# Kernel optimization log

Hardware: AMD Instinct MI355X
Metric: run time of the kernel (lower is better)

## Reference

```python
import jax, jax.numpy as jnp
import numpy as np

N = 50000       # num_nodes
E = 1_600_000   # num_edges (avg degree 32)
F_IN, HID, F_OUT = 128, 128, 64


def setup_inputs() -> dict:
    key = jax.random.key(0)
    k0, k1, k2, k3 = jax.random.split(key, 4)
    x = jax.random.normal(k0, (1, N, F_IN), dtype=jnp.float32)
    edge_index = jax.random.randint(k1, (2, E), 0, N, dtype=jnp.int32)
    # GCNConv weights (glorot-ish scale) and zero biases
    W1 = jax.random.normal(k2, (F_IN, HID), dtype=jnp.float32) / np.float32(np.sqrt(F_IN))
    b1 = jnp.zeros((HID,), dtype=jnp.float32)
    W2 = jax.random.normal(k3, (HID, F_OUT), dtype=jnp.float32) / np.float32(np.sqrt(HID))
    b2 = jnp.zeros((F_OUT,), dtype=jnp.float32)
    return {"x": x, "edge_index": edge_index, "W1": W1, "b1": b1, "W2": W2, "b2": b2}


def _gcn_layer(h, src, dst, norm, W, b, n):
    # linear transform then symmetric-normalized scatter-add aggregation
    h = h @ W                              # [N, F_out]
    msg = h[src] * norm[:, None]           # [E+N, F_out] gathered messages
    agg = jax.ops.segment_sum(msg, dst, num_segments=n)
    return agg + b


def reference(x, edge_index, W1, b1, W2, b2):
    xn = x[0]                              # [N, F_in] node feature matrix
    n = xn.shape[0]
    src, dst = edge_index[0], edge_index[1]
    # add self-loops (GCNConv default)
    loops = jnp.arange(n, dtype=src.dtype)
    src = jnp.concatenate([src, loops])
    dst = jnp.concatenate([dst, loops])
    # symmetric normalization: deg^-1/2[src] * deg^-1/2[dst] (deg >= 1 w/ self-loops)
    deg = jax.ops.segment_sum(jnp.ones(dst.shape, dtype=xn.dtype), dst, num_segments=n)
    dinv = jax.lax.rsqrt(deg)
    norm = dinv[src] * dinv[dst]
    h = jax.nn.relu(_gcn_layer(xn, src, dst, norm, W1, b1, n))
    out = jax.nn.relu(_gcn_layer(h, src, dst, norm, W2, b2, n))
    return out
```

## Files before the change

### kernel.cpp

```cpp
#include <hip/hip_runtime.h>
#include <hip/hip_fp16.h>


#define TILE 8192
#define BIN_CAP 2560

typedef _Float16 half8 __attribute__((ext_vector_type(8)));
typedef float floatx4 __attribute__((ext_vector_type(4)));

__device__ __forceinline__ void accs8(float* ax, const uint4& u, float d) {
    float2 f;
    f = __half22float2(*(const __half2*)&u.x); ax[0] = fmaf(d, f.x, ax[0]); ax[1] = fmaf(d, f.y, ax[1]);
    f = __half22float2(*(const __half2*)&u.y); ax[2] = fmaf(d, f.x, ax[2]); ax[3] = fmaf(d, f.y, ax[3]);
    f = __half22float2(*(const __half2*)&u.z); ax[4] = fmaf(d, f.x, ax[4]); ax[5] = fmaf(d, f.y, ax[5]);
    f = __half22float2(*(const __half2*)&u.w); ax[6] = fmaf(d, f.x, ax[6]); ax[7] = fmaf(d, f.y, ax[7]);
}

__device__ __forceinline__ void acc8(float* ax, const uint4& u) {
    float2 f;
    f = __half22float2(*(const __half2*)&u.x); ax[0] += f.x; ax[1] += f.y;
    f = __half22float2(*(const __half2*)&u.y); ax[2] += f.x; ax[3] += f.y;
    f = __half22float2(*(const __half2*)&u.z); ax[4] += f.x; ax[5] += f.y;
    f = __half22float2(*(const __half2*)&u.w); ax[6] += f.x; ax[7] += f.y;
}

template <int COLS>
__global__ __launch_bounds__(512) void bin_gemm(
        const int* __restrict__ src, const int* __restrict__ dst, int E,
        int nbins, int numTiles,
        int* __restrict__ binCnt, unsigned* __restrict__ recs,
        const float* __restrict__ Xv, const float* __restrict__ W,
        __half* __restrict__ Y, int N) {
    constexpr int LDA = 136;
    __shared__ __align__(16) _Float16 smem[(64 + COLS) * LDA];
    int tid = threadIdx.x;

    if (blockIdx.x < numTiles) {
        int* cnt = (int*)smem;
        int* gbase = cnt + nbins;
        for (int i = tid; i < nbins; i += 512) cnt[i] = 0;
        __syncthreads();

        int t0 = blockIdx.x * TILE;
        int tEnd = min(t0 + TILE, E);

        for (int e = t0 + tid; e < tEnd; e += 512)
            atomicAdd(&cnt[dst[e] >> 6], 1);
        __syncthreads();

        for (int i = tid; i < nbins; i += 512) {
            int c = cnt[i];
            gbase[i] = (c > 0) ? atomicAdd(&binCnt[i], c) : 0;
            cnt[i] = 0;
        }
        __syncthreads();

        for (int e = t0 + tid; e < tEnd; e += 512) {
            int d = dst[e];
            int s = src[e];
            int b = d >> 6;
            int r = atomicAdd(&cnt[b], 1);
            int g = gbase[b] + r;
            if (g < BIN_CAP)
                recs[(size_t)b * BIN_CAP + g] = ((unsigned)(d & 63) << 16) | (unsigned)s;
        }
        return;
    }

    int bid = blockIdx.x - numTiles;
    _Float16* aT = smem;
    _Float16* bT = smem + 64 * LDA;
    int lane = tid & 63, wave = tid >> 6;
    int row0 = bid * 64;

    for (int i = tid * 4; i < 64 * 128; i += 2048) {
        int r = i >> 7, k = i & 127;
        int gr = row0 + r;
        float4 v = make_float4(0.f, 0.f, 0.f, 0.f);
        if (gr < N) v = *(const float4*)&Xv[(size_t)gr * 128 + k];
        __half2 p0 = __floats2half2_rn(v.x, v.y);
        __half2 p1 = __floats2half2_rn(v.z, v.w);
        *(uint2*)&aT[r * LDA + k] = make_uint2(*(uint*)&p0, *(uint*)&p1);
    }
    for (int i = tid; i < 128 * COLS; i += 512) {
        int k = i / COLS, n = i % COLS;
        bT[n * LDA + k] = (_Float16)W[i];
    }
    __syncthreads();

    constexpr int NT = COLS / 16;
    int m = lane & 15, q = lane >> 4;
    floatx4 acc[NT];
    if (wave < 4) {
        #pragma unroll
        for (int t = 0; t < NT; t++) acc[t] = (floatx4){0.f, 0.f, 0.f, 0.f};
        const _Float16* arow = &aT[(wave * 16 + m) * LDA + q * 8];
        #pragma unroll
        for (int ks = 0; ks < 4; ks++) {
            half8 af = *(const half8*)&arow[ks * 32];
            #pragma unroll
            for (int t = 0; t < NT; t++) {
                half8 bf = *(const half8*)&bT[(t * 16 + m) * LDA + ks * 32 + q * 8];
                acc[t] = __builtin_amdgcn_mfma_f32_16x16x32_f16(af, bf, acc[t], 0, 0, 0);
            }
        }
    }
    __syncthreads();

    if (wave < 4) {
        #pragma unroll
        for (int t = 0; t < NT; t++)
            #pragma unroll
            for (int r = 0; r < 4; r++)
                aT[(wave * 16 + q * 4 + r) * LDA + t * 16 + m] = (_Float16)acc[t][r];
    }
    __syncthreads();

    for (int i = tid; i < 64 * (COLS / 2); i += 512) {
        int r = i / (COLS / 2), c = i % (COLS / 2);
        int gr = row0 + r;
        if (gr < N)
            ((uint*)Y)[(size_t)gr * (COLS / 2) + c] = *(uint*)&aT[r * LDA + c * 2];
    }
}

__global__ __launch_bounds__(512) void sort_bins(const unsigned* __restrict__ recs,
                                                 const int* __restrict__ binCnt,
                                                 unsigned short* __restrict__ sortedG,
                                                 int* __restrict__ startG,
                                                 float* __restrict__ dinv, int N) {
    __shared__ unsigned short sorted[BIN_CAP];
    __shared__ int c64[64];
    __shared__ int start[65];
    __shared__ int cursor[64];
    int b = blockIdx.x, tid = threadIdx.x;
    int lane = tid & 63, wave = tid >> 6;

    if (tid < 64) c64[tid] = 0;
    __syncthreads();
    int cnt = min(binCnt[b], BIN_CAP);
    const unsigned* bin = recs + (size_t)b * BIN_CAP;

    for (int i = tid; i < cnt; i += 512)
        atomicAdd(&c64[bin[i] >> 16], 1);
    __syncthreads();

    if (wave == 0) {
        int c = c64[lane];
        int v = c;
        #pragma unroll
        for (int off = 1; off < 64; off <<= 1) {
            int t = __shfl_up(v, off);
            if (lane >= off) v += t;
        }
        start[lane] = v - c;
        cursor[lane] = v - c;
        startG[b * 65 + lane] = v - c;
        if (lane == 63) { start[64] = v; startG[b * 65 + 64] = v; }
        int n = (b << 6) + lane;
        if (n < N) dinv[n] = rsqrtf((float)(c + 1));
    }
    __syncthreads();

    for (int i = tid; i < cnt; i += 512) {
        unsigned r = bin[i];
        int pos = atomicAdd(&cursor[r >> 16], 1);
        sorted[pos] = (unsigned short)(r & 0xFFFFu);
    }
    __syncthreads();
    unsigned short* sg = sortedG + (size_t)b * BIN_CAP;
    for (int i = tid; i < cnt; i += 512) sg[i] = sorted[i];
}

__global__ __launch_bounds__(512) void agg_gemm_fused(
        const __half* __restrict__ G,
        const unsigned short* __restrict__ sortedG,
        const int* __restrict__ startG,
        const float* __restrict__ dinv,
        const float* __restrict__ bias,
        const float* __restrict__ W2,
        __half* __restrict__ Y2, int N) {
    constexpr int LDH = 136;
    __shared__ unsigned short buf[BIN_CAP];
    __shared__ int st[65];
    __shared__ __align__(16) _Float16 hT[64 * LDH];
    __shared__ __align__(16) _Float16 bT[64 * LDH];

    int b = blockIdx.x;
    int tid = threadIdx.x, lane = tid & 63, wave = tid >> 6;
    int ql = lane & 15, quad = lane >> 4;

    if (tid < 65) st[tid] = startG[b * 65 + tid];
    __syncthreads();
    int cnt = st[64];
    const unsigned short* sg = sortedG + (size_t)b * BIN_CAP;
    for (int i = tid; i < cnt; i += 512) buf[i] = sg[i];
    for (int i = tid; i < 128 * 64; i += 512) {
        int k = i >> 6, n = i & 63;
        bT[n * LDH + k] = (_Float16)W2[i];
    }
    __syncthreads();

    float bb[8];
    #pragma unroll
    for (int k = 0; k < 4; k++) {
        float2 t = *(const float2*)&bias[ql * 8 + k * 2];
        bb[k * 2] = t.x; bb[k * 2 + 1] = t.y;
    }

    for (int rr = 0; rr < 8; rr++) {
        int row = wave * 8 + rr;
        int n = (b << 6) + row;
        if (n >= N) {
            if (quad == 0) {
                uint4 z = make_uint4(0, 0, 0, 0);
                *(uint4*)&hT[row * LDH + ql * 8] = z;
            }
            continue;
        }
        int jst = st[row], jen = st[row + 1];

        float ax[8] = {};
        int j = jst + quad;
        for (; j + 4 < jen; j += 8) {
            int sA = buf[j], sB = buf[j + 4];
            uint4 uA = *(const uint4*)&G[(size_t)sA * 128 + ql * 8];
            uint4 uB = *(const uint4*)&G[(size_t)sB * 128 + ql * 8];
            float dA = dinv[sA], dB = dinv[sB];
            accs8(ax, uA, dA);
            accs8(ax, uB, dB);
        }
        for (; j < jen; j += 4) {
            int s = buf[j];
            uint4 u = *(const uint4*)&G[(size_t)s * 128 + ql * 8];
            accs8(ax, u, dinv[s]);
        }
        #pragma unroll
        for (int k = 0; k < 8; k++) {
            ax[k] += __shfl_xor(ax[k], 16);
            ax[k] += __shfl_xor(ax[k], 32);
        }
        if (quad == 0) {
            uint4 us = *(const uint4*)&G[(size_t)n * 128 + ql * 8];
            float di = dinv[n];
            accs8(ax, us, di);
            __half2 h[4];
            #pragma unroll
            for (int k = 0; k < 4; k++) {
                float o0 = fmaxf(fmaf(di, ax[k * 2],     bb[k * 2]),     0.0f);
                float o1 = fmaxf(fmaf(di, ax[k * 2 + 1], bb[k * 2 + 1]), 0.0f);
                h[k] = __floats2half2_rn(o0, o1);
            }
            *(uint4*)&hT[row * LDH + ql * 8] = *(uint4*)h;
        }
    }
    __syncthreads();

    int m = lane & 15, q = lane >> 4;
    int mt = wave & 3, nt0 = (wave >> 2) * 2;
    floatx4 acc[2] = {(floatx4){0.f, 0.f, 0.f, 0.f}, (floatx4){0.f, 0.f, 0.f, 0.f}};
    const _Float16* arow = &hT[(mt * 16 + m) * LDH + q * 8];
    #pragma unroll
    for (int ks = 0; ks < 4; ks++) {
        half8 af = *(const half8*)&arow[ks * 32];
        #pragma unroll
        for (int t = 0; t < 2; t++) {
            half8 bf = *(const half8*)&bT[((nt0 + t) * 16 + m) * LDH + ks * 32 + q * 8];
            acc[t] = __builtin_amdgcn_mfma_f32_16x16x32_f16(af, bf, acc[t], 0, 0, 0);
        }
    }
    __syncthreads();

    float dv[4];
    #pragma unroll
    for (int r = 0; r < 4; r++) {
        int gr = (b << 6) + mt * 16 + q * 4 + r;
        dv[r] = (gr < N) ? dinv[gr] : 0.0f;
    }
    #pragma unroll
    for (int t = 0; t < 2; t++)
        #pragma unroll
        for (int r = 0; r < 4; r++)
            hT[(mt * 16 + q * 4 + r) * LDH + (nt0 + t) * 16 + m] = (_Float16)(dv[r] * acc[t][r]);
    __syncthreads();

    for (int i = tid; i < 64 * 32; i += 512) {
        int r = i >> 5, c = i & 31;
        int gr = (b << 6) + r;
        if (gr < N)
            ((uint*)Y2)[(size_t)gr * 32 + c] = *(uint*)&hT[r * LDH + c * 2];
    }
}

__global__ __launch_bounds__(512) void agg_64(const __half* __restrict__ G,
                                              const unsigned short* __restrict__ sortedG,
                                              const int* __restrict__ startG,
                                              const float* __restrict__ dinv,
                                              const float* __restrict__ bias,
                                              float* __restrict__ out, int N) {
    __shared__ unsigned short buf[BIN_CAP];
    __shared__ int st[33];
    int b = blockIdx.x, half_ = blockIdx.y;
    int tid = threadIdx.x, lane = tid & 63, wave = tid >> 6;
    int ol = lane & 7, oct = lane >> 3;
    int r0 = half_ * 32;

    if (tid < 33) st[tid] = startG[b * 65 + r0 + tid];
    __syncthreads();
    int S0 = st[0], S1 = st[32];
    const unsigned short* sg = sortedG + (size_t)b * BIN_CAP;
    for (int i = tid; i < S1 - S0; i += 512) buf[i] = sg[S0 + i];
    __syncthreads();

    float bb[8];
    #pragma unroll
    for (int k = 0; k < 4; k++) {
        float2 t = *(const float2*)&bias[ol * 8 + k * 2];
        bb[k * 2] = t.x; bb[k * 2 + 1] = t.y;
    }

    for (int rr = 0; rr < 4; rr++) {
        int row = wave * 4 + rr;
        int n = (b << 6) + r0 + row;
        if (n >= N) continue;
        int jst = st[row] - S0, jen = st[row + 1] - S0;

        float ax[8] = {};
        int j = jst + oct;
        for (; j + 8 < jen; j += 16) {
            int sA = buf[j], sB = buf[j + 8];
            uint4 uA = *(const uint4*)&G[(size_t)sA * 64 + ol * 8];
            uint4 uB = *(const uint4*)&G[(size_t)sB * 64 + ol * 8];
            acc8(ax, uA);
            acc8(ax, uB);
        }
        for (; j < jen; j += 8) {
            int s = buf[j];
            uint4 u = *(const uint4*)&G[(size_t)s * 64 + ol * 8];
            acc8(ax, u);
        }
        #pragma unroll
        for (int k = 0; k < 8; k++) {
            ax[k] += __shfl_xor(ax[k], 8);
            ax[k] += __shfl_xor(ax[k], 16);
            ax[k] += __shfl_xor(ax[k], 32);
        }
        if (oct < 2) {
            uint4 us = *(const uint4*)&G[(size_t)n * 64 + ol * 8];
            acc8(ax, us);
            float di = dinv[n];
            float o[8];
            #pragma unroll
            for (int k = 0; k < 8; k++)
                o[k] = fmaxf(fmaf(di, ax[k], bb[k]), 0.0f);
            if (oct == 0)
                *(float4*)&out[(size_t)n * 64 + ol * 8] = make_float4(o[0], o[1], o[2], o[3]);
            else
                *(float4*)&out[(size_t)n * 64 + ol * 8 + 4] = make_float4(o[4], o[5], o[6], o[7]);
        }
    }
}

extern "C" void kernel_launch(void* const* d_in, const int* in_sizes, int n_in,
                              void* d_out, int out_size, void* d_ws, size_t ws_size,
                              hipStream_t stream) {
    const float* x  = (const float*)d_in[0];
    const int*   ei = (const int*)d_in[1];
    const float* W1 = (const float*)d_in[2];
    const float* b1 = (const float*)d_in[3];
    const float* W2 = (const float*)d_in[4];
    const float* b2 = (const float*)d_in[5];
    float* out = (float*)d_out;

    const int HID  = in_sizes[3];
    const int F_IN = in_sizes[2] / HID;
    const int N    = in_sizes[0] / F_IN;
    const int E    = in_sizes[1] / 2;
    (void)n_in; (void)out_size; (void)ws_size; (void)F_IN;

    const int* src = ei;
    const int* dst = ei + E;

    const int nbins = (N + 63) >> 6;

    char* p = (char*)d_ws;
    auto carve = [&](size_t bytes) { void* q = (void*)p; p += (bytes + 255) & ~(size_t)255; return q; };
    int*            binCnt  = (int*)           carve((size_t)nbins * 4);
    float*          dinv    = (float*)         carve((size_t)N * 4);
    unsigned*       recs    = (unsigned*)      carve((size_t)nbins * BIN_CAP * 4);
    unsigned short* sortedG = (unsigned short*)carve((size_t)nbins * BIN_CAP * 2);
    int*            startG  = (int*)           carve((size_t)nbins * 65 * 4);
    __half*         bufG    = (__half*)        carve((size_t)N * 128 * 2);
    __half*         bufG2   = (__half*)        carve((size_t)N * 64 * 2);

    hipMemsetAsync(binCnt, 0, (size_t)nbins * 4, stream);

    int numTiles = (E + TILE - 1) / TILE;
    int gemmGrid = (N + 63) / 64;
    bin_gemm<128><<<numTiles + gemmGrid, 512, 0, stream>>>(
        src, dst, E, nbins, numTiles, binCnt, recs, x, W1, bufG, N);

    sort_bins<<<nbins, 512, 0, stream>>>(recs, binCnt, sortedG, startG, dinv, N);

    agg_gemm_fused<<<nbins, 512, 0, stream>>>(bufG, sortedG, startG, dinv, b1, W2, bufG2, N);

    dim3 aggGrid(nbins, 2);
    agg_64<<<aggGrid, 512, 0, stream>>>(bufG2, sortedG, startG, dinv, b2, out, N);
}
```

Baseline: 205.2 us.

## Prescale layer-1 features by source dinv using a separate degree-count kernel

Adds a kernel that counts in-degrees with global atomics before the first GEMM, so the GEMM epilogue can multiply each output row by its source-side rsqrt(deg+1). The layer-1 aggregation loop then only sums the gathered fp16 rows, with no per-edge dinv gather and no FMA by it. The cost is an extra launch and a pass over E edges with about 1.6M global atomics, plus a rounding change because the scaling is applied before the fp16 conversion.

```diff
diff --git a/kernel.cpp b/kernel.cpp
--- a/kernel.cpp
+++ b/kernel.cpp
@@ -7,14 +7,6 @@
 
 typedef _Float16 half8 __attribute__((ext_vector_type(8)));
 typedef float floatx4 __attribute__((ext_vector_type(4)));
-
-__device__ __forceinline__ void accs8(float* ax, const uint4& u, float d) {
-    float2 f;
-    f = __half22float2(*(const __half2*)&u.x); ax[0] = fmaf(d, f.x, ax[0]); ax[1] = fmaf(d, f.y, ax[1]);
-    f = __half22float2(*(const __half2*)&u.y); ax[2] = fmaf(d, f.x, ax[2]); ax[3] = fmaf(d, f.y, ax[3]);
-    f = __half22float2(*(const __half2*)&u.z); ax[4] = fmaf(d, f.x, ax[4]); ax[5] = fmaf(d, f.y, ax[5]);
-    f = __half22float2(*(const __half2*)&u.w); ax[6] = fmaf(d, f.x, ax[6]); ax[7] = fmaf(d, f.y, ax[7]);
-}
 
 __device__ __forceinline__ void acc8(float* ax, const uint4& u) {
     float2 f;
@@ -24,12 +16,34 @@
     f = __half22float2(*(const __half2*)&u.w); ax[6] += f.x; ax[7] += f.y;
 }
 
+template <bool VEC>
+__global__ __launch_bounds__(512) void deg_count(const int* __restrict__ dst, int E,
+                                                 int* __restrict__ deg) {
+    if (VEC) {
+        int nv = E >> 2;
+        const int4* d4 = (const int4*)dst;
+        for (int k = blockIdx.x * 512 + threadIdx.x; k < nv; k += gridDim.x * 512) {
+            int4 d = d4[k];
+            atomicAdd(&deg[d.x], 1);
+            atomicAdd(&deg[d.y], 1);
+            atomicAdd(&deg[d.z], 1);
+            atomicAdd(&deg[d.w], 1);
+        }
+        if (blockIdx.x == 0 && (int)threadIdx.x < (E & 3))
+            atomicAdd(&deg[dst[(nv << 2) + threadIdx.x]], 1);
+    } else {
+        for (int e = blockIdx.x * 512 + threadIdx.x; e < E; e += gridDim.x * 512)
+            atomicAdd(&deg[dst[e]], 1);
+    }
+}
+
 template <int COLS>
 __global__ __launch_bounds__(512) void bin_gemm(
         const int* __restrict__ src, const int* __restrict__ dst, int E,
         int nbins, int numTiles,
         int* __restrict__ binCnt, unsigned* __restrict__ recs,
         const float* __restrict__ Xv, const float* __restrict__ W,
+        const int* __restrict__ deg,
         __half* __restrict__ Y, int N) {
     constexpr int LDA = 136;
     __shared__ __align__(16) _Float16 smem[(64 + COLS) * LDA];
@@ -108,11 +122,17 @@
     __syncthreads();
 
     if (wave < 4) {
+        float dv[4];
+        #pragma unroll
+        for (int r = 0; r < 4; r++) {
+            int gr = row0 + wave * 16 + q * 4 + r;
+            dv[r] = (gr < N) ? rsqrtf((float)(deg[gr] + 1)) : 0.0f;
+        }
         #pragma unroll
         for (int t = 0; t < NT; t++)
             #pragma unroll
             for (int r = 0; r < 4; r++)
-                aT[(wave * 16 + q * 4 + r) * LDA + t * 16 + m] = (_Float16)acc[t][r];
+                aT[(wave * 16 + q * 4 + r) * LDA + t * 16 + m] = (_Float16)(dv[r] * acc[t][r]);
     }
     __syncthreads();
 
@@ -226,14 +246,13 @@
             int sA = buf[j], sB = buf[j + 4];
             uint4 uA = *(const uint4*)&G[(size_t)sA * 128 + ql * 8];
             uint4 uB = *(const uint4*)&G[(size_t)sB * 128 + ql * 8];
-            float dA = dinv[sA], dB = dinv[sB];
-            accs8(ax, uA, dA);
-            accs8(ax, uB, dB);
+            acc8(ax, uA);
+            acc8(ax, uB);
         }
         for (; j < jen; j += 4) {
             int s = buf[j];
             uint4 u = *(const uint4*)&G[(size_t)s * 128 + ql * 8];
-            accs8(ax, u, dinv[s]);
+            acc8(ax, u);
         }
         #pragma unroll
         for (int k = 0; k < 8; k++) {
@@ -242,8 +261,8 @@
         }
         if (quad == 0) {
             uint4 us = *(const uint4*)&G[(size_t)n * 128 + ql * 8];
+            acc8(ax, us);
             float di = dinv[n];
-            accs8(ax, us, di);
             __half2 h[4];
             #pragma unroll
             for (int k = 0; k < 4; k++) {
@@ -386,6 +405,7 @@
     char* p = (char*)d_ws;
     auto carve = [&](size_t bytes) { void* q = (void*)p; p += (bytes + 255) & ~(size_t)255; return q; };
     int*            binCnt  = (int*)           carve((size_t)nbins * 4);
+    int*            deg     = (int*)           carve((size_t)N * 4);
     float*          dinv    = (float*)         carve((size_t)N * 4);
     unsigned*       recs    = (unsigned*)      carve((size_t)nbins * BIN_CAP * 4);
     unsigned short* sortedG = (unsigned short*)carve((size_t)nbins * BIN_CAP * 2);
@@ -393,12 +413,25 @@
     __half*         bufG    = (__half*)        carve((size_t)N * 128 * 2);
     __half*         bufG2   = (__half*)        carve((size_t)N * 64 * 2);
 
-    hipMemsetAsync(binCnt, 0, (size_t)nbins * 4, stream);
+    size_t zeroBytes = (size_t)((char*)dinv - (char*)binCnt);
+    hipMemsetAsync(binCnt, 0, zeroBytes, stream);
+
+    bool vec = ((reinterpret_cast<uintptr_t>(dst) & 15) == 0) && ((E & 3) == 0 || E >= 4);
+    if (vec) {
+        int nv = E >> 2;
+        int dblocks = min((nv + 511) / 512, 1024);
+        if (dblocks < 1) dblocks = 1;
+        deg_count<true><<<dblocks, 512, 0, stream>>>(dst, E, deg);
+    } else {
+        int dblocks = min((E + 511) / 512, 2048);
+        if (dblocks < 1) dblocks = 1;
+        deg_count<false><<<dblocks, 512, 0, stream>>>(dst, E, deg);
+    }
 
     int numTiles = (E + TILE - 1) / TILE;
     int gemmGrid = (N + 63) / 64;
     bin_gemm<128><<<numTiles + gemmGrid, 512, 0, stream>>>(
-        src, dst, E, nbins, numTiles, binCnt, recs, x, W1, bufG, N);
+        src, dst, E, nbins, numTiles, binCnt, recs, x, W1, deg, bufG, N);
 
     sort_bins<<<nbins, 512, 0, stream>>>(recs, binCnt, sortedG, startG, dinv, N);
 
```

Measured after the change: 275.9 us. 1.34x slower.

## Fuse GCN pipeline into a single cooperative persistent kernel with grid syncs

Applied to the files above, without the earlier changes.

Replaces the memset plus four separate launches with one cooperative kernel of nbins blocks that runs binning, the first GEMM, bin sorting, dinv-scaled store, fused aggregation+GEMM and final aggregation, separated by grid-wide syncs. The first GEMM result is held in registers across the sort phase and pre-scaled by dinv before storing, and the last aggregation uses a different wave layout. The aim is to remove launch gaps and tail effects between stages. The cost is grid-sync overhead, an occupancy requirement of 782 co-resident blocks, and lower parallelism in the final stage (one block per bin instead of two). A fallback to the old multi-kernel path is kept when cooperative launch capacity is insufficient.

```diff
diff --git a/kernel.cpp b/kernel.cpp
--- a/kernel.cpp
+++ b/kernel.cpp
@@ -1,5 +1,8 @@
 #include <hip/hip_runtime.h>
 #include <hip/hip_fp16.h>
+#include <hip/hip_cooperative_groups.h>
+
+namespace cg = cooperative_groups;
 
 
 #define TILE 8192
@@ -7,6 +10,14 @@
 
 typedef _Float16 half8 __attribute__((ext_vector_type(8)));
 typedef float floatx4 __attribute__((ext_vector_type(4)));
+
+__device__ __forceinline__ void acc8(float* ax, const uint4& u) {
+    float2 f;
+    f = __half22float2(*(const __half2*)&u.x); ax[0] += f.x; ax[1] += f.y;
+    f = __half22float2(*(const __half2*)&u.y); ax[2] += f.x; ax[3] += f.y;
+    f = __half22float2(*(const __half2*)&u.z); ax[4] += f.x; ax[5] += f.y;
+    f = __half22float2(*(const __half2*)&u.w); ax[6] += f.x; ax[7] += f.y;
+}
 
 __device__ __forceinline__ void accs8(float* ax, const uint4& u, float d) {
     float2 f;
@@ -16,16 +27,334 @@
     f = __half22float2(*(const __half2*)&u.w); ax[6] = fmaf(d, f.x, ax[6]); ax[7] = fmaf(d, f.y, ax[7]);
 }
 
-__device__ __forceinline__ void acc8(float* ax, const uint4& u) {
-    float2 f;
-    f = __half22float2(*(const __half2*)&u.x); ax[0] += f.x; ax[1] += f.y;
-    f = __half22float2(*(const __half2*)&u.y); ax[2] += f.x; ax[3] += f.y;
-    f = __half22float2(*(const __half2*)&u.z); ax[4] += f.x; ax[5] += f.y;
-    f = __half22float2(*(const __half2*)&u.w); ax[6] += f.x; ax[7] += f.y;
+__global__ __launch_bounds__(512, 8) void mega_gcn(
+        const int* __restrict__ src, const int* __restrict__ dst, int E,
+        int nbins, int numTiles,
+        int* __restrict__ binCnt, unsigned* __restrict__ recs,
+        const float* __restrict__ Xv, const float* __restrict__ W1,
+        unsigned short* __restrict__ sortedG, int* __restrict__ startG,
+        float* __restrict__ dinv,
+        const float* __restrict__ b1, const float* __restrict__ W2,
+        __half* __restrict__ bufG, __half* __restrict__ bufG2,
+        const float* __restrict__ b2, float* __restrict__ out, int N) {
+    __shared__ __align__(16) char L[40448];
+    cg::grid_group gridg = cg::this_grid();
+    int bid = blockIdx.x, tid = threadIdx.x;
+    int lane = tid & 63, wave = tid >> 6;
+
+    for (int i = bid * 512 + tid; i < nbins; i += gridDim.x * 512) binCnt[i] = 0;
+    gridg.sync();
+
+    if (bid < numTiles) {
+        int* cnt = (int*)L;
+        int* gbase = cnt + nbins;
+        for (int i = tid; i < nbins; i += 512) cnt[i] = 0;
+        __syncthreads();
+        int t0 = bid * TILE, tEnd = min(t0 + TILE, E);
+        for (int e = t0 + tid; e < tEnd; e += 512)
+            atomicAdd(&cnt[dst[e] >> 6], 1);
+        __syncthreads();
+        for (int i = tid; i < nbins; i += 512) {
+            int c = cnt[i];
+            gbase[i] = (c > 0) ? atomicAdd(&binCnt[i], c) : 0;
+            cnt[i] = 0;
+        }
+        __syncthreads();
+        for (int e = t0 + tid; e < tEnd; e += 512) {
+            int d = dst[e], s = src[e];
+            int b = d >> 6;
+            int r = atomicAdd(&cnt[b], 1);
+            int g = gbase[b] + r;
+            if (g < BIN_CAP)
+                recs[(size_t)b * BIN_CAP + g] = ((unsigned)(d & 63) << 16) | (unsigned)s;
+        }
+        __syncthreads();
+    }
+
+    int gtile = bid + (nbins - numTiles);
+    if (gtile >= nbins) gtile -= nbins;
+    int row0g = gtile * 64;
+    floatx4 accg[8];
+    #pragma unroll
+    for (int t = 0; t < 8; t++) accg[t] = (floatx4){0.f, 0.f, 0.f, 0.f};
+    {
+        _Float16* aT  = (_Float16*)L;
+        _Float16* bTh = (_Float16*)(L + 17408);
+        for (int i = tid * 4; i < 64 * 128; i += 2048) {
+            int r = i >> 7, k = i & 127;
+            int gr = row0g + r;
+            float4 v = make_float4(0.f, 0.f, 0.f, 0.f);
+            if (gr < N) v = *(const float4*)&Xv[(size_t)gr * 128 + k];
+            __half2 p0 = __floats2half2_rn(v.x, v.y);
+            __half2 p1 = __floats2half2_rn(v.z, v.w);
+            *(uint2*)&aT[r * 136 + k] = make_uint2(*(uint*)&p0, *(uint*)&p1);
+        }
+        int m = lane & 15, q = lane >> 4;
+        #pragma unroll
+        for (int h = 0; h < 2; h++) {
+            __syncthreads();
+            for (int i = tid; i < 128 * 64; i += 512) {
+                int k = i >> 6, n = i & 63;
+                bTh[n * 136 + k] = (_Float16)W1[k * 128 + h * 64 + n];
+            }
+            __syncthreads();
+            if (wave < 4) {
+                const _Float16* arow = &aT[(wave * 16 + m) * 136 + q * 8];
+                #pragma unroll
+                for (int ks = 0; ks < 4; ks++) {
+                    half8 af = *(const half8*)&arow[ks * 32];
+                    #pragma unroll
+                    for (int t = 0; t < 4; t++) {
+                        half8 bf = *(const half8*)&bTh[(t * 16 + m) * 136 + ks * 32 + q * 8];
+                        accg[h * 4 + t] = __builtin_amdgcn_mfma_f32_16x16x32_f16(
+                            af, bf, accg[h * 4 + t], 0, 0, 0);
+                    }
+                }
+            }
+        }
+    }
+    gridg.sync();
+
+    {
+        unsigned short* sorted = (unsigned short*)L;
+        int* c64    = (int*)(L + 5120);
+        int* cursor = (int*)(L + 5648);
+        if (tid < 64) c64[tid] = 0;
+        __syncthreads();
+        int cnt = min(binCnt[bid], BIN_CAP);
+        const unsigned* bin = recs + (size_t)bid * BIN_CAP;
+        for (int i = tid; i < cnt; i += 512)
+            atomicAdd(&c64[bin[i] >> 16], 1);
+        __syncthreads();
+        if (wave == 0) {
+            int c = c64[lane];
+            int v = c;
+            #pragma unroll
+            for (int off = 1; off < 64; off <<= 1) {
+                int t = __shfl_up(v, off);
+                if (lane >= off) v += t;
+            }
+            cursor[lane] = v - c;
+            startG[bid * 65 + lane] = v - c;
+            if (lane == 63) startG[bid * 65 + 64] = v;
+            int n = (bid << 6) + lane;
+            if (n < N) dinv[n] = rsqrtf((float)(c + 1));
+        }
+        __syncthreads();
+        for (int i = tid; i < cnt; i += 512) {
+            unsigned r = bin[i];
+            int pos = atomicAdd(&cursor[r >> 16], 1);
+            sorted[pos] = (unsigned short)(r & 0xFFFFu);
+        }
+        __syncthreads();
+        unsigned short* sg = sortedG + (size_t)bid * BIN_CAP;
+        for (int i = tid; i < cnt; i += 512) sg[i] = sorted[i];
+    }
+    gridg.sync();
+
+    {
+        _Float16* bounce = (_Float16*)L;
+        int m = lane & 15, q = lane >> 4;
+        if (wave < 4) {
+            float dv[4];
+            #pragma unroll
+            for (int r = 0; r < 4; r++) {
+                int gr = row0g + wave * 16 + q * 4 + r;
+                dv[r] = (gr < N) ? dinv[gr] : 0.0f;
+            }
+            #pragma unroll
+            for (int h = 0; h < 2; h++)
+                #pragma unroll
+                for (int t = 0; t < 4; t++)
+                    #pragma unroll
+                    for (int r = 0; r < 4; r++)
+                        bounce[(wave * 16 + q * 4 + r) * 136 + h * 64 + t * 16 + m] =
+                            (_Float16)(dv[r] * accg[h * 4 + t][r]);
+        }
+        __syncthreads();
+        for (int i = tid; i < 64 * 64; i += 512) {
+            int r = i >> 6, c = i & 63;
+            int gr = row0g + r;
+            if (gr < N)
+                ((uint*)bufG)[(size_t)gr * 64 + c] = *(uint*)&bounce[r * 136 + c * 2];
+        }
+    }
+    gridg.sync();
+
+    {
+        constexpr int LDH = 136;
+        unsigned short* buf = (unsigned short*)L;
+        int* st = (int*)(L + 5120);
+        _Float16* hT = (_Float16*)(L + 5408);
+        _Float16* bT = (_Float16*)(L + 22816);
+        int ql = lane & 15, quad = lane >> 4;
+
+        if (tid < 65) st[tid] = startG[bid * 65 + tid];
+        __syncthreads();
+        int cnt = st[64];
+        const unsigned short* sg = sortedG + (size_t)bid * BIN_CAP;
+        for (int i = tid; i < cnt; i += 512) buf[i] = sg[i];
+        for (int i = tid; i < 128 * 64; i += 512) {
+            int k = i >> 6, n = i & 63;
+            bT[n * LDH + k] = (_Float16)W2[i];
+        }
+        __syncthreads();
+
+        float bb[8];
+        #pragma unroll
+        for (int k = 0; k < 4; k++) {
+            float2 t = *(const float2*)&b1[ql * 8 + k * 2];
+            bb[k * 2] = t.x; bb[k * 2 + 1] = t.y;
+        }
+
+        const __half* G = bufG;
+        for (int rr = 0; rr < 8; rr++) {
+            int row = wave * 8 + rr;
+            int n = (bid << 6) + row;
+            if (n >= N) {
+                if (quad == 0) {
+                    uint4 z = make_uint4(0, 0, 0, 0);
+                    *(uint4*)&hT[row * LDH + ql * 8] = z;
+                }
+                continue;
+            }
+            int jst = st[row], jen = st[row + 1];
+            float ax[8] = {};
+            int j = jst + quad;
+            for (; j + 4 < jen; j += 8) {
+                int sA = buf[j], sB = buf[j + 4];
+                uint4 uA = *(const uint4*)&G[(size_t)sA * 128 + ql * 8];
+                uint4 uB = *(const uint4*)&G[(size_t)sB * 128 + ql * 8];
+                acc8(ax, uA);
+                acc8(ax, uB);
+            }
+            for (; j < jen; j += 4) {
+                int s = buf[j];
+                uint4 u = *(const uint4*)&G[(size_t)s * 128 + ql * 8];
+                acc8(ax, u);
+            }
+            #pragma unroll
+            for (int k = 0; k < 8; k++) {
+                ax[k] += __shfl_xor(ax[k], 16);
+                ax[k] += __shfl_xor(ax[k], 32);
+            }
+            if (quad == 0) {
+                uint4 us = *(const uint4*)&G[(size_t)n * 128 + ql * 8];
+                acc8(ax, us);
+                float di = dinv[n];
+                __half2 h[4];
+                #pragma unroll
+                for (int k = 0; k < 4; k++) {
+                    float o0 = fmaxf(fmaf(di, ax[k * 2],     bb[k * 2]),     0.0f);
+                    float o1 = fmaxf(fmaf(di, ax[k * 2 + 1], bb[k * 2 + 1]), 0.0f);
+                    h[k] = __floats2half2_rn(o0, o1);
+                }
+                *(uint4*)&hT[row * LDH + ql * 8] = *(uint4*)h;
+            }
+        }
+        __syncthreads();
+
+        int m = lane & 15, q = lane >> 4;
+        int mt = wave & 3, nt0 = (wave >> 2) * 2;
+        floatx4 acc[2] = {(floatx4){0.f, 0.f, 0.f, 0.f}, (floatx4){0.f, 0.f, 0.f, 0.f}};
+        const _Float16* arow = &hT[(mt * 16 + m) * LDH + q * 8];
+        #pragma unroll
+        for (int ks = 0; ks < 4; ks++) {
+            half8 af = *(const half8*)&arow[ks * 32];
+            #pragma unroll
+            for (int t = 0; t < 2; t++) {
+                half8 bf = *(const half8*)&bT[((nt0 + t) * 16 + m) * LDH + ks * 32 + q * 8];
+                acc[t] = __builtin_amdgcn_mfma_f32_16x16x32_f16(af, bf, acc[t], 0, 0, 0);
+            }
+        }
+        __syncthreads();
+
+        float dv[4];
+        #pragma unroll
+        for (int r = 0; r < 4; r++) {
+            int gr = (bid << 6) + mt * 16 + q * 4 + r;
+            dv[r] = (gr < N) ? dinv[gr] : 0.0f;
+        }
+        #pragma unroll
+        for (int t = 0; t < 2; t++)
+            #pragma unroll
+            for (int r = 0; r < 4; r++)
+                hT[(mt * 16 + q * 4 + r) * LDH + (nt0 + t) * 16 + m] = (_Float16)(dv[r] * acc[t][r]);
+        __syncthreads();
+
+        for (int i = tid; i < 64 * 32; i += 512) {
+            int r = i >> 5, c = i & 31;
+            int gr = (bid << 6) + r;
+            if (gr < N)
+                ((uint*)bufG2)[(size_t)gr * 32 + c] = *(uint*)&hT[r * LDH + c * 2];
+        }
+    }
+    gridg.sync();
+
+    {
+        unsigned short* buf = (unsigned short*)L;
+        int* st = (int*)(L + 5120);
+        int ol = lane & 7, oct = lane >> 3;
+
+        if (tid < 65) st[tid] = startG[bid * 65 + tid];
+        __syncthreads();
+        int cnt = st[64];
+        const unsigned short* sg = sortedG + (size_t)bid * BIN_CAP;
+        for (int i = tid; i < cnt; i += 512) buf[i] = sg[i];
+        __syncthreads();
+
+        float bb[8];
+        #pragma unroll
+        for (int k = 0; k < 4; k++) {
+            float2 t = *(const float2*)&b2[ol * 8 + k * 2];
+            bb[k * 2] = t.x; bb[k * 2 + 1] = t.y;
+        }
+
+        const __half* G = bufG2;
+        for (int rr = 0; rr < 8; rr++) {
+            int row = wave * 8 + rr;
+            int n = (bid << 6) + row;
+            if (n >= N) continue;
+            int jst = st[row], jen = st[row + 1];
+            float ax[8] = {};
+            int j = jst + oct;
+            for (; j + 8 < jen; j += 16) {
+                int sA = buf[j], sB = buf[j + 8];
+                uint4 uA = *(const uint4*)&G[(size_t)sA * 64 + ol * 8];
+                uint4 uB = *(const uint4*)&G[(size_t)sB * 64 + ol * 8];
+                acc8(ax, uA);
+                acc8(ax, uB);
+            }
+            for (; j < jen; j += 8) {
+                int s = buf[j];
+                uint4 u = *(const uint4*)&G[(size_t)s * 64 + ol * 8];
+                acc8(ax, u);
+            }
+            #pragma unroll
+            for (int k = 0; k < 8; k++) {
+                ax[k] += __shfl_xor(ax[k], 8);
+                ax[k] += __shfl_xor(ax[k], 16);
+                ax[k] += __shfl_xor(ax[k], 32);
+            }
+            if (oct < 2) {
+                uint4 us = *(const uint4*)&G[(size_t)n * 64 + ol * 8];
+                acc8(ax, us);
+                float di = dinv[n];
+                float o[8];
+                #pragma unroll
+                for (int k = 0; k < 8; k++)
+                    o[k] = fmaxf(fmaf(di, ax[k], bb[k]), 0.0f);
+                if (oct == 0)
+                    *(float4*)&out[(size_t)n * 64 + ol * 8] = make_float4(o[0], o[1], o[2], o[3]);
+                else
+                    *(float4*)&out[(size_t)n * 64 + ol * 8 + 4] = make_float4(o[4], o[5], o[6], o[7]);
+            }
+        }
+    }
 }
 
 template <int COLS>
-__global__ __launch_bounds__(512) void bin_gemm(
+__global__ __launch_bounds__(512) void fb_bin_gemm(
         const int* __restrict__ src, const int* __restrict__ dst, int E,
         int nbins, int numTiles,
         int* __restrict__ binCnt, unsigned* __restrict__ recs,
@@ -40,24 +369,19 @@
         int* gbase = cnt + nbins;
         for (int i = tid; i < nbins; i += 512) cnt[i] = 0;
         __syncthreads();
-
         int t0 = blockIdx.x * TILE;
         int tEnd = min(t0 + TILE, E);
-
         for (int e = t0 + tid; e < tEnd; e += 512)
             atomicAdd(&cnt[dst[e] >> 6], 1);
         __syncthreads();
-
         for (int i = tid; i < nbins; i += 512) {
             int c = cnt[i];
             gbase[i] = (c > 0) ? atomicAdd(&binCnt[i], c) : 0;
             cnt[i] = 0;
         }
         __syncthreads();
-
         for (int e = t0 + tid; e < tEnd; e += 512) {
-            int d = dst[e];
-            int s = src[e];
+            int d = dst[e], s = src[e];
             int b = d >> 6;
             int r = atomicAdd(&cnt[b], 1);
             int g = gbase[b] + r;
@@ -106,7 +430,6 @@
         }
     }
     __syncthreads();
-
     if (wave < 4) {
         #pragma unroll
         for (int t = 0; t < NT; t++)
@@ -115,7 +438,6 @@
                 aT[(wave * 16 + q * 4 + r) * LDA + t * 16 + m] = (_Float16)acc[t][r];
     }
     __syncthreads();
-
     for (int i = tid; i < 64 * (COLS / 2); i += 512) {
         int r = i / (COLS / 2), c = i % (COLS / 2);
         int gr = row0 + r;
@@ -124,14 +446,13 @@
     }
 }
 
-__global__ __launch_bounds__(512) void sort_bins(const unsigned* __restrict__ recs,
-                                                 const int* __restrict__ binCnt,
-                                                 unsigned short* __restrict__ sortedG,
-                                                 int* __restrict__ startG,
-                                                 float* __restrict__ dinv, int N) {
+__global__ __launch_bounds__(512) void fb_sort_bins(const unsigned* __restrict__ recs,
+                                                    const int* __restrict__ binCnt,
+                                                    unsigned short* __restrict__ sortedG,
+                                                    int* __restrict__ startG,
+                                                    float* __restrict__ dinv, int N) {
     __shared__ unsigned short sorted[BIN_CAP];
     __shared__ int c64[64];
-    __shared__ int start[65];
     __shared__ int cursor[64];
     int b = blockIdx.x, tid = threadIdx.x;
     int lane = tid & 63, wave = tid >> 6;
@@ -140,11 +461,9 @@
     __syncthreads();
     int cnt = min(binCnt[b], BIN_CAP);
     const unsigned* bin = recs + (size_t)b * BIN_CAP;
-
     for (int i = tid; i < cnt; i += 512)
         atomicAdd(&c64[bin[i] >> 16], 1);
     __syncthreads();
-
     if (wave == 0) {
         int c = c64[lane];
         int v = c;
@@ -153,15 +472,13 @@
             int t = __shfl_up(v, off);
             if (lane >= off) v += t;
         }
-        start[lane] = v - c;
         cursor[lane] = v - c;
         startG[b * 65 + lane] = v - c;
-        if (lane == 63) { start[64] = v; startG[b * 65 + 64] = v; }
+        if (lane == 63) startG[b * 65 + 64] = v;
         int n = (b << 6) + lane;
         if (n < N) dinv[n] = rsqrtf((float)(c + 1));
     }
     __syncthreads();
-
     for (int i = tid; i < cnt; i += 512) {
         unsigned r = bin[i];
         int pos = atomicAdd(&cursor[r >> 16], 1);
@@ -172,7 +489,7 @@
     for (int i = tid; i < cnt; i += 512) sg[i] = sorted[i];
 }
 
-__global__ __launch_bounds__(512) void agg_gemm_fused(
+__global__ __launch_bounds__(512) void fb_agg_gemm_fused(
         const __half* __restrict__ G,
         const unsigned short* __restrict__ sortedG,
         const int* __restrict__ startG,
@@ -219,7 +536,6 @@
             continue;
         }
         int jst = st[row], jen = st[row + 1];
-
         float ax[8] = {};
         int j = jst + quad;
         for (; j + 4 < jen; j += 8) {
@@ -292,12 +608,12 @@
     }
 }
 
-__global__ __launch_bounds__(512) void agg_64(const __half* __restrict__ G,
-                                              const unsigned short* __restrict__ sortedG,
-                                              const int* __restrict__ startG,
-                                              const float* __restrict__ dinv,
-                                              const float* __restrict__ bias,
-                                              float* __restrict__ out, int N) {
+__global__ __launch_bounds__(512) void fb_agg_64(const __half* __restrict__ G,
+                                                 const unsigned short* __restrict__ sortedG,
+                                                 const int* __restrict__ startG,
+                                                 const float* __restrict__ dinv,
+                                                 const float* __restrict__ bias,
+                                                 float* __restrict__ out, int N) {
     __shared__ unsigned short buf[BIN_CAP];
     __shared__ int st[33];
     int b = blockIdx.x, half_ = blockIdx.y;
@@ -324,7 +640,6 @@
         int n = (b << 6) + r0 + row;
         if (n >= N) continue;
         int jst = st[row] - S0, jen = st[row + 1] - S0;
-
         float ax[8] = {};
         int j = jst + oct;
         for (; j + 8 < jen; j += 16) {
@@ -382,6 +697,8 @@
     const int* dst = ei + E;
 
     const int nbins = (N + 63) >> 6;
+    int numTiles = (E + TILE - 1) / TILE;
+    int gemmGrid = (N + 63) / 64;
 
     char* p = (char*)d_ws;
     auto carve = [&](size_t bytes) { void* q = (void*)p; p += (bytes + 255) & ~(size_t)255; return q; };
@@ -393,17 +710,35 @@
     __half*         bufG    = (__half*)        carve((size_t)N * 128 * 2);
     __half*         bufG2   = (__half*)        carve((size_t)N * 64 * 2);
 
-    hipMemsetAsync(binCnt, 0, (size_t)nbins * 4, stream);
-
-    int numTiles = (E + TILE - 1) / TILE;
-    int gemmGrid = (N + 63) / 64;
-    bin_gemm<128><<<numTiles + gemmGrid, 512, 0, stream>>>(
-        src, dst, E, nbins, numTiles, binCnt, recs, x, W1, bufG, N);
-
-    sort_bins<<<nbins, 512, 0, stream>>>(recs, binCnt, sortedG, startG, dinv, N);
-
-    agg_gemm_fused<<<nbins, 512, 0, stream>>>(bufG, sortedG, startG, dinv, b1, W2, bufG2, N);
-
-    dim3 aggGrid(nbins, 2);
-    agg_64<<<aggGrid, 512, 0, stream>>>(bufG2, sortedG, startG, dinv, b2, out, N);
+    static int s_cap = -1;
+    if (s_cap < 0) {
+        hipDeviceProp_t prop;
+        int mab = 0, cap = 0;
+        if (hipGetDeviceProperties(&prop, 0) == hipSuccess && prop.cooperativeLaunch) {
+            if (hipOccupancyMaxActiveBlocksPerMultiprocessor(&mab, mega_gcn, 512, 0) == hipSuccess)
+                cap = mab * prop.multiProcessorCount;
+        }
+        s_cap = cap;
+    }
+
+    bool useMega = (s_cap >= nbins) && (gemmGrid == nbins) &&
+                   (numTiles <= nbins) && ((size_t)nbins * 8 <= 40448);
+
+    if (useMega) {
+        void* args[] = {
+            (void*)&src, (void*)&dst, (void*)&E, (void*)&nbins, (void*)&numTiles,
+            (void*)&binCnt, (void*)&recs, (void*)&x, (void*)&W1,
+            (void*)&sortedG, (void*)&startG, (void*)&dinv,
+            (void*)&b1, (void*)&W2, (void*)&bufG, (void*)&bufG2,
+            (void*)&b2, (void*)&out, (void*)&N};
+        hipLaunchCooperativeKernel(mega_gcn, dim3(nbins), dim3(512), args, 0, stream);
+    } else {
+        hipMemsetAsync(binCnt, 0, (size_t)nbins * 4, stream);
+        fb_bin_gemm<128><<<numTiles + gemmGrid, 512, 0, stream>>>(
+            src, dst, E, nbins, numTiles, binCnt, recs, x, W1, bufG, N);
+        fb_sort_bins<<<nbins, 512, 0, stream>>>(recs, binCnt, sortedG, startG, dinv, N);
+        fb_agg_gemm_fused<<<nbins, 512, 0, stream>>>(bufG, sortedG, startG, dinv, b1, W2, bufG2, N);
+        dim3 aggGrid(nbins, 2);
+        fb_agg_64<<<aggGrid, 512, 0, stream>>>(bufG2, sortedG, startG, dinv, b2, out, N);
+    }
 }
```

New measurement: 212.3 us. 3.4% more time.
